# Performance work log

Hardware: AMD Instinct MI355X
Metric: run time of the kernel (lower is better)

## Reference

```python
import jax, jax.numpy as jnp
import numpy as np

N_CLASSES = 10


def setup_inputs() -> dict:
    key = jax.random.key(0)
    k1, k2, k3 = jax.random.split(key, 3)
    x_test = jax.random.uniform(k1, (2048, 784), dtype=jnp.float32)
    x_train = jax.random.uniform(k2, (50000, 784), dtype=jnp.float32)
    y_train = jax.random.randint(k3, (50000,), 0, N_CLASSES, dtype=jnp.int64)
    return {"x_test": x_test, "x_train": x_train, "y_train": y_train, "k": 5}


def reference(x_test, x_train, y_train, k):
    B = x_test.shape[0]
    xt = x_test.reshape(B, -1)                      # [B, D]
    xdb = x_train.reshape(x_train.shape[0], -1)     # [N, D]
    # similarity: matches on 1s + matches on 0s (binary-pixel Hamming-like score)
    dist_full = xt @ xdb.T + (1.0 - xt) @ (1.0 - xdb).T   # [B, N]
    _, idx = jax.lax.top_k(dist_full, k)            # [B, k] nearest-neighbor indices
    yk = y_train[idx]                               # [B, k] neighbor labels
    # per-row mode vote; argmax over class-count histogram == torch's
    counts = jnp.sum(jax.nn.one_hot(yk, N_CLASSES, dtype=jnp.int32), axis=1)  # [B, C]
    return jnp.argmax(counts, axis=1)
```

## Files before the change

kernel.cpp:

```cpp
#include <hip/hip_runtime.h>
#include <float.h>
#include <stdint.h>

#define D_DIM 784
#define KPADB 832
#define N_TRAIN 50000
#define NPAD 50048
#define B_TEST 2048
#define N_CLASSES 10
#define TOPK 5
#define NBLK 391
#define SEL 8
#define SBIAS 12645136
#define NT 13

typedef __attribute__((ext_vector_type(4))) int int4v;

__device__ inline unsigned umax32(unsigned a, unsigned b) { return a > b ? a : b; }

__device__ inline void ins8(unsigned long long* tk, unsigned long long v) {
    #pragma unroll
    for (int s = 0; s < SEL; ++s) {
        unsigned long long mx = v > tk[s] ? v : tk[s];
        unsigned long long mn = v > tk[s] ? tk[s] : v;
        tk[s] = mx; v = mn;
    }
}

__device__ inline void ins5u(unsigned* tk, unsigned v) {
    #pragma unroll
    for (int s = 0; s < TOPK; ++s) {
        unsigned mx = v > tk[s] ? v : tk[s];
        unsigned mn = v > tk[s] ? tk[s] : v;
        tk[s] = mx; v = mn;
    }
}

#define INSERT5(tvarr, tiarr, CV, CI)                                   \
    {                                                                   \
        float _cv = (CV); int _ci = (CI);                               \
        _Pragma("unroll")                                               \
        for (int _s = 0; _s < TOPK; ++_s) {                             \
            bool _bet = (_cv > tvarr[_s]) ||                            \
                        (_cv == tvarr[_s] && _ci < tiarr[_s]);          \
            float _fv = _bet ? tvarr[_s] : _cv;                         \
            int   _fi = _bet ? tiarr[_s] : _ci;                         \
            tvarr[_s] = _bet ? _cv : tvarr[_s];                         \
            tiarr[_s] = _bet ? _ci : tiarr[_s];                         \
            _cv = _fv; _ci = _fi;                                       \
        }                                                               \
    }

__device__ inline unsigned pack4q(float4 f) {
    int q0 = __float2int_rn(fmaf(f.x, 254.f, -127.f));
    int q1 = __float2int_rn(fmaf(f.y, 254.f, -127.f));
    int q2 = __float2int_rn(fmaf(f.z, 254.f, -127.f));
    int q3 = __float2int_rn(fmaf(f.w, 254.f, -127.f));
    return (unsigned)(q0 & 255) | ((unsigned)(q1 & 255) << 8) |
           ((unsigned)(q2 & 255) << 16) | ((unsigned)(q3 & 255) << 24);
}

__global__ __launch_bounds__(256)
void quant_kernel(const float* __restrict__ xtr, const float* __restrict__ xte,
                  char* __restrict__ Bq, char* __restrict__ Aq) {
    const int blk = blockIdx.x;
    const float* src;
    char* dst;
    int rows_src, row;
    if (blk < NPAD / 4) {
        src = xtr; dst = Bq; rows_src = N_TRAIN;
        row = blk * 4 + (threadIdx.x >> 6);
    } else {
        src = xte; dst = Aq; rows_src = B_TEST;
        row = (blk - NPAD / 4) * 4 + (threadIdx.x >> 6);
        if (row >= B_TEST) return;
    }
    const int lane = threadIdx.x & 63;
    if (lane >= 52) return;
    uint4 w = {0u, 0u, 0u, 0u};
    if (row < rows_src && lane < 49) {
        const float4* p = (const float4*)(src + (size_t)row * D_DIM + lane * 16);
        w.x = pack4q(p[0]);
        w.y = pack4q(p[1]);
        w.z = pack4q(p[2]);
        w.w = pack4q(p[3]);
    }
    *(uint4*)(dst + (size_t)row * KPADB + lane * 16) = w;
}

__global__ __launch_bounds__(256, 4)
void knn_mfma(const char* __restrict__ Aq, const char* __restrict__ Bq,
              unsigned* __restrict__ cval) {
    const int bid = blockIdx.x;
    const int xcd = bid & 7;
    const int sidx = bid >> 3;
    const int st_g = (sidx >> 4) * 8 + xcd;
    const int r16 = sidx & 15;
    const int mblk = (st_g & 3) * 4 + (r16 & 3);
    const int nchunk = (st_g >> 2) * 4 + (r16 >> 2);
    if (nchunk >= NBLK) return;

    __shared__ char lds_raw[39936] __attribute__((aligned(16)));
    unsigned* epi  = (unsigned*)lds_raw;
    unsigned* lval = (unsigned*)(lds_raw + 34816);

    const int tid = threadIdx.x;
    const int w = tid >> 6, lane = tid & 63;
    const int l15 = lane & 15, q = lane >> 4;
    const int mb = mblk * 128, nb = nchunk * 128;
    const int mw = (w & 1) * 64, nw = (w >> 1) * 64;

    const int s_tile = w >> 1, s_half = w & 1;
    const char* sbase = (s_tile == 0) ? (Aq + (size_t)mb * KPADB)
                                      : (Bq + (size_t)nb * KPADB);
    const char* srow = sbase + (size_t)s_half * 64 * KPADB;
    const int ldsw_off = s_tile * 8192 + s_half * 4096;

    int choff[4];
    #pragma unroll
    for (int c = 0; c < 4; ++c) {
        int s = c * 64 + lane;
        int rl = s >> 2;
        int k4 = (s & 3) ^ ((rl >> 1) & 3);
        choff[c] = rl * KPADB + k4 * 16;
    }
    const int ch = (q ^ ((l15 >> 1) & 3)) * 16;
    int aoff[4], boff[4];
    #pragma unroll
    for (int i = 0; i < 4; ++i) {
        aoff[i] = (mw + i * 16 + l15) * 64 + ch;
        boff[i] = (nw + i * 16 + l15) * 64 + ch;
    }

    int4v acc[4][4];
    #pragma unroll
    for (int i = 0; i < 4; ++i)
        #pragma unroll
        for (int j = 0; j < 4; ++j)
            acc[i][j] = (int4v){0, 0, 0, 0};

    #define STAGE_TILE(BUF, KT)                                               \
        {                                                                     \
            char* dst_ = lds_raw + (BUF) * 16384 + ldsw_off;                  \
            _Pragma("unroll")                                                 \
            for (int c_ = 0; c_ < 4; ++c_) {                                  \
                __builtin_amdgcn_global_load_lds(                             \
                    (const __attribute__((address_space(1))) void*)           \
                        (srow + choff[c_] + (KT)),                            \
                    (__attribute__((address_space(3))) void*)(dst_ + c_ * 1024),\
                    16, 0, 0);                                                \
            }                                                                 \
        }

    #define COMPUTE_TILE(BUF)                                                 \
        {                                                                     \
            const char* ab_ = lds_raw + (BUF) * 16384;                        \
            int4v a_[4], b_[4];                                               \
            _Pragma("unroll")                                                 \
            for (int i_ = 0; i_ < 4; ++i_) a_[i_] = *(const int4v*)(ab_ + aoff[i_]); \
            _Pragma("unroll")                                                 \
            for (int j_ = 0; j_ < 4; ++j_) b_[j_] = *(const int4v*)(ab_ + 8192 + boff[j_]); \
            _Pragma("unroll")                                                 \
            for (int i_ = 0; i_ < 4; ++i_)                                    \
                _Pragma("unroll")                                             \
                for (int j_ = 0; j_ < 4; ++j_)                                \
                    acc[i_][j_] = __builtin_amdgcn_mfma_i32_16x16x64_i8(      \
                        a_[i_], b_[j_], acc[i_][j_], 0, 0, 0);                \
        }

    STAGE_TILE(0, 0);
    __syncthreads();
    for (int t = 0; t < NT - 1; ++t) {
        const int cur = t & 1;
        STAGE_TILE(cur ^ 1, (t + 1) * 64);
        __builtin_amdgcn_sched_barrier(0);
        COMPUTE_TILE(cur);
        __syncthreads();
    }
    COMPUTE_TILE(0);

    int okn[4];
    #pragma unroll
    for (int j = 0; j < 4; ++j) okn[j] = (nb + nw + j * 16 + l15 < N_TRAIN);

    for (int h = 0; h < 2; ++h) {
        __syncthreads();
        if ((w & 1) == h) {
            #pragma unroll
            for (int i = 0; i < 4; ++i) {
                int r = i * 16 + q * 4;
                #pragma unroll
                for (int j = 0; j < 4; ++j) {
                    int col = nw + j * 16 + l15;
                    uint4 kv;
                    if (okn[j]) {
                        int4v s = acc[i][j];
                        kv.x = ((unsigned)(s.x + SBIAS) << 7) | (unsigned)col;
                        kv.y = ((unsigned)(s.y + SBIAS) << 7) | (unsigned)col;
                        kv.z = ((unsigned)(s.z + SBIAS) << 7) | (unsigned)col;
                        kv.w = ((unsigned)(s.w + SBIAS) << 7) | (unsigned)col;
                    } else {
                        kv.x = kv.y = kv.z = kv.w = (unsigned)col;
                    }
                    *(uint4*)(epi + col * 68 + r) = kv;
                }
            }
        }
        __syncthreads();
        {
            int r = tid & 63, qq = tid >> 6;
            const unsigned* ebase = epi + (qq * 32) * 68 + r;
            unsigned tv5[TOPK] = {0u, 0u, 0u, 0u, 0u};
            #pragma unroll
            for (int c = 0; c < 32; ++c) ins5u(tv5, ebase[c * 68]);
            #pragma unroll
            for (int s = 0; s < TOPK; ++s) lval[(r * 4 + qq) * TOPK + s] = tv5[s];
        }
        __syncthreads();
        if (tid < 64) {
            unsigned tv[TOPK] = {0u, 0u, 0u, 0u, 0u};
            for (int qq = 0; qq < 4; ++qq)
                #pragma unroll
                for (int s = 0; s < TOPK; ++s) {
                    unsigned cv = lval[(tid * 4 + qq) * TOPK + s];
                    if (cv > tv[TOPK - 1]) ins5u(tv, cv);
                }
            int grow = mb + h * 64 + tid;
            size_t base = ((size_t)grow * NBLK + nchunk) * TOPK;
            #pragma unroll
            for (int s = 0; s < TOPK; ++s) cval[base + s] = tv[s];
        }
    }
    #undef STAGE_TILE
    #undef COMPUTE_TILE
}

__global__ __launch_bounds__(256)
void knn_final(const unsigned* __restrict__ cval,
               const float* __restrict__ xt, const float* __restrict__ xtr,
               const int* __restrict__ y, int* __restrict__ out) {
    __shared__ unsigned long long sv[256][SEL];
    __shared__ double cs[SEL];
    __shared__ int    cn[SEL];
    const int b = blockIdx.x;
    const int t = threadIdx.x;

    unsigned long long tk[SEL];
    #pragma unroll
    for (int s = 0; s < SEL; ++s) tk[s] = 0ull;

    const unsigned* row = cval + (size_t)b * (NBLK * TOPK);
    for (int e = t; e < NBLK * TOPK; e += 256) {
        unsigned v = row[e];
        int chunk = e / TOPK;
        unsigned n = (unsigned)chunk * 128u + (v & 127u);
        unsigned long long v64 = ((unsigned long long)v << 16) | n;
        if (v64 > tk[SEL - 1]) ins8(tk, v64);
    }
    #pragma unroll
    for (int s = 0; s < SEL; ++s) sv[t][s] = tk[s];
    __syncthreads();

    for (int off = 128; off >= 1; off >>= 1) {
        if (t < off) {
            if (sv[t + off][0] > tk[SEL - 1]) {
                #pragma unroll
                for (int s = 0; s < SEL; ++s) {
                    unsigned long long v = sv[t + off][s];
                    if (v > tk[SEL - 1]) ins8(tk, v);
                }
                #pragma unroll
                for (int s = 0; s < SEL; ++s) sv[t][s] = tk[s];
            }
        }
        __syncthreads();
    }

    const int w = t >> 6, lane = t & 63, half = lane >> 5, hl = lane & 31;
    const int c = w * 2 + half;
    {
        int n = (int)(sv[0][c] & 0xFFFFull);
        double dot = 0.0, rs = 0.0;
        if (n < N_TRAIN) {
            const float4* pa = (const float4*)(xt + (size_t)b * D_DIM);
            const float4* pb = (const float4*)(xtr + (size_t)n * D_DIM);
            #pragma unroll
            for (int jj = 0; jj < 7; ++jj) {
                int j = hl + jj * 32;
                if (j < 196) {
                    float4 a = pa[j], bb = pb[j];
                    dot += (double)a.x * bb.x + (double)a.y * bb.y +
                           (double)a.z * bb.z + (double)a.w * bb.w;
                    rs  += (double)bb.x + (double)bb.y + (double)bb.z + (double)bb.w;
                }
            }
        }
        #pragma unroll
        for (int off = 16; off > 0; off >>= 1) {
            dot += __shfl_down(dot, off, 32);
            rs  += __shfl_down(rs, off, 32);
        }
        if (hl == 0) {
            cs[c] = (n < N_TRAIN) ? (2.0 * dot - rs) : -1.0e300;
            cn[c] = n;
        }
    }
    __syncthreads();

    if (t == 0) {
        double bv[TOPK]; int bi[TOPK];
        #pragma unroll
        for (int s = 0; s < TOPK; ++s) { bv[s] = -1.0e300; bi[s] = 0x7fffffff; }
        for (int cc = 0; cc < SEL; ++cc) {
            double cv = cs[cc]; int ci = cn[cc];
            #pragma unroll
            for (int s = 0; s < TOPK; ++s) {
                bool bet = (cv > bv[s]) || (cv == bv[s] && ci < bi[s]);
                double fv = bet ? bv[s] : cv;
                int    fi = bet ? bi[s] : ci;
                bv[s] = bet ? cv : bv[s];
                bi[s] = bet ? ci : bi[s];
                cv = fv; ci = fi;
            }
        }
        int lab[TOPK];
        #pragma unroll
        for (int s = 0; s < TOPK; ++s) lab[s] = y[bi[s]];
        int best_c = 0, best_cnt = -1;
        #pragma unroll
        for (int cc = 0; cc < N_CLASSES; ++cc) {
            int cnt = 0;
            #pragma unroll
            for (int s = 0; s < TOPK; ++s) cnt += (lab[s] == cc) ? 1 : 0;
            if (cnt > best_cnt) { best_cnt = cnt; best_c = cc; }
        }
        out[b] = best_c;
    }
}

#define FBM 64
#define FBN 64
#define FBK 16
#define FNCH 32
#define FCHUNK 1600

__global__ __launch_bounds__(256)
void rowsum_kernel(const float* __restrict__ x, float* __restrict__ s) {
    int row = blockIdx.x * 4 + (threadIdx.x >> 6);
    int lane = threadIdx.x & 63;
    if (row >= N_TRAIN) return;
    const float* p = x + (size_t)row * D_DIM;
    float acc = 0.f;
    for (int i = lane; i < D_DIM; i += 64) acc += p[i];
    #pragma unroll
    for (int off = 32; off > 0; off >>= 1) acc += __shfl_down(acc, off, 64);
    if (lane == 0) s[row] = acc;
}

__global__ __launch_bounds__(256)
void knn_phaseA_fb(const float* __restrict__ xt, const float* __restrict__ xtr,
                   const float* __restrict__ strain,
                   float* __restrict__ cval, int* __restrict__ cidx) {
    __shared__ float As[FBK][FBM + 4];
    __shared__ float Bs[FBK][FBN + 4];
    __shared__ float lv[FBM][16][TOPK];
    __shared__ int   li[FBM][16][TOPK];

    const int tid = threadIdx.x;
    const int tx = tid & 15, ty = tid >> 4;
    const int b0 = blockIdx.x * FBM;
    const int chunk = blockIdx.y;
    const int n_base = chunk * FCHUNK;
    const int lrow = tid >> 2;
    const int lk4  = (tid & 3) * 4;

    float tv[4][TOPK]; int ti[4][TOPK];
    #pragma unroll
    for (int i = 0; i < 4; ++i)
        #pragma unroll
        for (int s = 0; s < TOPK; ++s) { tv[i][s] = -FLT_MAX; ti[i][s] = 0x7fffffff; }

    for (int nt = 0; nt < FCHUNK; nt += FBN) {
        const int n0 = n_base + nt;
        double accd[4][4];
        #pragma unroll
        for (int i = 0; i < 4; ++i)
            #pragma unroll
            for (int j = 0; j < 4; ++j) accd[i][j] = 0.0;

        for (int kt = 0; kt < D_DIM; kt += FBK) {
            float4 av = *(const float4*)(xt + (size_t)(b0 + lrow) * D_DIM + kt + lk4);
            As[lk4 + 0][lrow] = av.x; As[lk4 + 1][lrow] = av.y;
            As[lk4 + 2][lrow] = av.z; As[lk4 + 3][lrow] = av.w;
            int nr = n0 + lrow;
            float4 bv = make_float4(0.f, 0.f, 0.f, 0.f);
            if (nr < N_TRAIN) bv = *(const float4*)(xtr + (size_t)nr * D_DIM + kt + lk4);
            Bs[lk4 + 0][lrow] = bv.x; Bs[lk4 + 1][lrow] = bv.y;
            Bs[lk4 + 2][lrow] = bv.z; Bs[lk4 + 3][lrow] = bv.w;
            __syncthreads();

            float accf[4][4] = {{0.f}};
            #pragma unroll
            for (int k = 0; k < FBK; ++k) {
                float a[4], b[4];
                #pragma unroll
                for (int i = 0; i < 4; ++i) a[i] = As[k][ty * 4 + i];
                #pragma unroll
                for (int j = 0; j < 4; ++j) b[j] = Bs[k][tx * 4 + j];
                #pragma unroll
                for (int i = 0; i < 4; ++i)
                    #pragma unroll
                    for (int j = 0; j < 4; ++j) accf[i][j] += a[i] * b[j];
            }
            #pragma unroll
            for (int i = 0; i < 4; ++i)
                #pragma unroll
                for (int j = 0; j < 4; ++j) accd[i][j] += (double)accf[i][j];
            __syncthreads();
        }

        #pragma unroll
        for (int j = 0; j < 4; ++j) {
            int n = n0 + tx * 4 + j;
            if (n < N_TRAIN) {
                float sn = strain[n];
                #pragma unroll
                for (int i = 0; i < 4; ++i) {
                    float sc = (float)(2.0 * accd[i][j] - (double)sn);
                    if (sc > tv[i][TOPK - 1] ||
                        (sc == tv[i][TOPK - 1] && n < ti[i][TOPK - 1])) {
                        INSERT5(tv[i], ti[i], sc, n);
                    }
                }
            }
        }
    }

    #pragma unroll
    for (int i = 0; i < 4; ++i)
        #pragma unroll
        for (int s = 0; s < TOPK; ++s) {
            lv[ty * 4 + i][tx][s] = tv[i][s];
            li[ty * 4 + i][tx][s] = ti[i][s];
        }
    __syncthreads();

    if (tid < FBM) {
        float bv5[TOPK]; int bi5[TOPK];
        #pragma unroll
        for (int s = 0; s < TOPK; ++s) { bv5[s] = -FLT_MAX; bi5[s] = 0x7fffffff; }
        for (int tt = 0; tt < 16; ++tt)
            #pragma unroll
            for (int s = 0; s < TOPK; ++s) {
                float cv = lv[tid][tt][s]; int ci = li[tid][tt][s];
                if (cv > bv5[TOPK - 1] || (cv == bv5[TOPK - 1] && ci < bi5[TOPK - 1])) {
                    INSERT5(bv5, bi5, cv, ci);
                }
            }
        size_t base = ((size_t)(b0 + tid) * FNCH + chunk) * TOPK;
        #pragma unroll
        for (int s = 0; s < TOPK; ++s) { cval[base + s] = bv5[s]; cidx[base + s] = bi5[s]; }
    }
}

__global__ __launch_bounds__(256)
void knn_phaseB_fb(const float* __restrict__ cval, const int* __restrict__ cidx,
                   const int* __restrict__ y, int* __restrict__ out) {
    int b = blockIdx.x * blockDim.x + threadIdx.x;
    if (b >= B_TEST) return;
    const float* v = cval + (size_t)b * FNCH * TOPK;
    const int* ix = cidx + (size_t)b * FNCH * TOPK;
    float bv5[TOPK]; int bi5[TOPK];
    #pragma unroll
    for (int s = 0; s < TOPK; ++s) { bv5[s] = -FLT_MAX; bi5[s] = 0x7fffffff; }
    for (int tt = 0; tt < FNCH * TOPK; ++tt) {
        float cv = v[tt]; int ci = ix[tt];
        if (cv > bv5[TOPK - 1] || (cv == bv5[TOPK - 1] && ci < bi5[TOPK - 1])) {
            INSERT5(bv5, bi5, cv, ci);
        }
    }
    int lab[TOPK];
    #pragma unroll
    for (int s = 0; s < TOPK; ++s) lab[s] = y[bi5[s]];
    int best_c = 0, best_cnt = -1;
    #pragma unroll
    for (int cc = 0; cc < N_CLASSES; ++cc) {
        int cnt = 0;
        #pragma unroll
        for (int s = 0; s < TOPK; ++s) cnt += (lab[s] == cc) ? 1 : 0;
        if (cnt > best_cnt) { best_cnt = cnt; best_c = cc; }
    }
    out[b] = best_c;
}

extern "C" void kernel_launch(void* const* d_in, const int* in_sizes, int n_in,
                              void* d_out, int out_size, void* d_ws, size_t ws_size,
                              hipStream_t stream) {
    const float* x_test  = (const float*)d_in[0];
    const float* x_train = (const float*)d_in[1];
    const int*   y_train = (const int*)d_in[2];
    int* out = (int*)d_out;

    const size_t sz_Bq  = (size_t)NPAD * KPADB;
    const size_t off_Aq = sz_Bq;
    const size_t sz_Aq  = (size_t)B_TEST * KPADB;
    const size_t off_cv = off_Aq + sz_Aq;
    const size_t sz_cv  = (size_t)B_TEST * NBLK * TOPK * 4;
    const size_t need   = off_cv + sz_cv;

    char* ws = (char*)d_ws;

    if (ws_size >= need) {
        char* Bq = ws;
        char* Aq = ws + off_Aq;
        unsigned* cval = (unsigned*)(ws + off_cv);

        quant_kernel<<<NPAD / 4 + B_TEST / 4, 256, 0, stream>>>(
            x_train, x_test, Bq, Aq);

        knn_mfma<<<6272, 256, 0, stream>>>(Aq, Bq, cval);

        knn_final<<<B_TEST, 256, 0, stream>>>(cval, x_test, x_train, y_train, out);
    } else {
        float* strain = (float*)ws;
        rowsum_kernel<<<N_TRAIN / 4, 256, 0, stream>>>(x_train, strain);
        float* cval = (float*)(ws + 200192);
        int*   cidx = (int*)(ws + 200192 + (size_t)B_TEST * FNCH * TOPK * 4);

        dim3 gridA(B_TEST / FBM, FNCH);
        knn_phaseA_fb<<<gridA, 256, 0, stream>>>(x_test, x_train, strain, cval, cidx);
        knn_phaseB_fb<<<(B_TEST + 255) / 256, 256, 0, stream>>>(cval, cidx, y_train, out);
    }
}
```

Measured before the change: 390.3 us.

## Load MFMA operands directly from global into registers, drop LDS staging

Replaces the LDS double-buffered global_load_lds staging with direct per-lane global loads into register double buffers (aX/bX, aY/bY) feeding the int8 MFMAs, fully unrolling the K loop. Launch bounds occupancy hint is lowered from 4 to 3 to allow more registers for the extra operand buffers. This removes LDS traffic and the per-tile barriers, but each wave now fetches its A/B rows from global/L2 itself, so data is no longer shared across waves. That raises global load volume and exposes latency.

Result: slower. 480.5 us (+23.1%).

```diff
diff --git a/kernel.cpp b/kernel.cpp
--- a/kernel.cpp
+++ b/kernel.cpp
@@ -88,7 +88,7 @@
     *(uint4*)(dst + (size_t)row * KPADB + lane * 16) = w;
 }
 
-__global__ __launch_bounds__(256, 4)
+__global__ __launch_bounds__(256, 3)
 void knn_mfma(const char* __restrict__ Aq, const char* __restrict__ Bq,
               unsigned* __restrict__ cval) {
     const int bid = blockIdx.x;
@@ -110,26 +110,12 @@
     const int mb = mblk * 128, nb = nchunk * 128;
     const int mw = (w & 1) * 64, nw = (w >> 1) * 64;
 
-    const int s_tile = w >> 1, s_half = w & 1;
-    const char* sbase = (s_tile == 0) ? (Aq + (size_t)mb * KPADB)
-                                      : (Bq + (size_t)nb * KPADB);
-    const char* srow = sbase + (size_t)s_half * 64 * KPADB;
-    const int ldsw_off = s_tile * 8192 + s_half * 4096;
-
-    int choff[4];
-    #pragma unroll
-    for (int c = 0; c < 4; ++c) {
-        int s = c * 64 + lane;
-        int rl = s >> 2;
-        int k4 = (s & 3) ^ ((rl >> 1) & 3);
-        choff[c] = rl * KPADB + k4 * 16;
-    }
-    const int ch = (q ^ ((l15 >> 1) & 3)) * 16;
-    int aoff[4], boff[4];
+    const char* apt[4];
+    const char* bpt[4];
     #pragma unroll
     for (int i = 0; i < 4; ++i) {
-        aoff[i] = (mw + i * 16 + l15) * 64 + ch;
-        boff[i] = (nw + i * 16 + l15) * 64 + ch;
+        apt[i] = Aq + (size_t)(mb + mw + i * 16 + l15) * KPADB + q * 16;
+        bpt[i] = Bq + (size_t)(nb + nw + i * 16 + l15) * KPADB + q * 16;
     }
 
     int4v acc[4][4];
@@ -139,45 +125,37 @@
         for (int j = 0; j < 4; ++j)
             acc[i][j] = (int4v){0, 0, 0, 0};
 
-    #define STAGE_TILE(BUF, KT)                                               \
+    #define LD8(DA, DB, KT)                                                   \
         {                                                                     \
-            char* dst_ = lds_raw + (BUF) * 16384 + ldsw_off;                  \
             _Pragma("unroll")                                                 \
-            for (int c_ = 0; c_ < 4; ++c_) {                                  \
-                __builtin_amdgcn_global_load_lds(                             \
-                    (const __attribute__((address_space(1))) void*)           \
-                        (srow + choff[c_] + (KT)),                            \
-                    (__attribute__((address_space(3))) void*)(dst_ + c_ * 1024),\
-                    16, 0, 0);                                                \
-            }                                                                 \
-        }
-
-    #define COMPUTE_TILE(BUF)                                                 \
+            for (int i_ = 0; i_ < 4; ++i_) DA[i_] = *(const int4v*)(apt[i_] + (KT)); \
+            _Pragma("unroll")                                                 \
+            for (int j_ = 0; j_ < 4; ++j_) DB[j_] = *(const int4v*)(bpt[j_] + (KT)); \
+        }
+    #define FMA16(SA, SB)                                                     \
         {                                                                     \
-            const char* ab_ = lds_raw + (BUF) * 16384;                        \
-            int4v a_[4], b_[4];                                               \
-            _Pragma("unroll")                                                 \
-            for (int i_ = 0; i_ < 4; ++i_) a_[i_] = *(const int4v*)(ab_ + aoff[i_]); \
-            _Pragma("unroll")                                                 \
-            for (int j_ = 0; j_ < 4; ++j_) b_[j_] = *(const int4v*)(ab_ + 8192 + boff[j_]); \
             _Pragma("unroll")                                                 \
             for (int i_ = 0; i_ < 4; ++i_)                                    \
                 _Pragma("unroll")                                             \
                 for (int j_ = 0; j_ < 4; ++j_)                                \
                     acc[i_][j_] = __builtin_amdgcn_mfma_i32_16x16x64_i8(      \
-                        a_[i_], b_[j_], acc[i_][j_], 0, 0, 0);                \
-        }
-
-    STAGE_TILE(0, 0);
-    __syncthreads();
-    for (int t = 0; t < NT - 1; ++t) {
-        const int cur = t & 1;
-        STAGE_TILE(cur ^ 1, (t + 1) * 64);
-        __builtin_amdgcn_sched_barrier(0);
-        COMPUTE_TILE(cur);
-        __syncthreads();
-    }
-    COMPUTE_TILE(0);
+                        SA[i_], SB[j_], acc[i_][j_], 0, 0, 0);                \
+        }
+
+    {
+        int4v aX[4], bX[4], aY[4], bY[4];
+        LD8(aX, bX, 0);
+        #pragma unroll
+        for (int t = 0; t < NT - 1; t += 2) {
+            LD8(aY, bY, (t + 1) * 64);
+            FMA16(aX, bX);
+            LD8(aX, bX, (t + 2) * 64);
+            FMA16(aY, bY);
+        }
+        FMA16(aX, bX);
+    }
+    #undef LD8
+    #undef FMA16
 
     int okn[4];
     #pragma unroll
@@ -231,8 +209,6 @@
             for (int s = 0; s < TOPK; ++s) cval[base + s] = tv[s];
         }
     }
-    #undef STAGE_TILE
-    #undef COMPUTE_TILE
 }
 
 __global__ __launch_bounds__(256)
```

## Triple-buffer MFMA K-loop with explicit vmcnt waits and dense quant threads

Applied to the files above, without the earlier changes.

Replaces the double-buffered int8 MFMA K-loop with a three-stage LDS ring, prefetching two tiles ahead, using explicit vmcnt waits and raw barriers, and raising wave priority around the MFMA burst. LDS grows to 48KB and launch bounds drop to 3 blocks per CU, trading occupancy for deeper load/compute overlap. The quantization kernel is reorganised so every thread handles one 16-byte chunk, removing the idle lanes of the old 64-lane-per-row mapping.

Result: no change. 394.0 us (+0.9%).

```diff
diff --git a/kernel.cpp b/kernel.cpp
--- a/kernel.cpp
+++ b/kernel.cpp
@@ -13,6 +13,7 @@
 #define SEL 8
 #define SBIAS 12645136
 #define NT 13
+#define RCHUNK 52
 
 typedef __attribute__((ext_vector_type(4))) int int4v;
 
@@ -63,32 +64,30 @@
 __global__ __launch_bounds__(256)
 void quant_kernel(const float* __restrict__ xtr, const float* __restrict__ xte,
                   char* __restrict__ Bq, char* __restrict__ Aq) {
-    const int blk = blockIdx.x;
+    unsigned c = blockIdx.x * 256 + threadIdx.x;
+    unsigned row = c / RCHUNK;
+    unsigned wc  = c - row * RCHUNK;
     const float* src;
     char* dst;
-    int rows_src, row;
-    if (blk < NPAD / 4) {
+    unsigned rows_src;
+    if (row < NPAD) {
         src = xtr; dst = Bq; rows_src = N_TRAIN;
-        row = blk * 4 + (threadIdx.x >> 6);
     } else {
+        row -= NPAD;
         src = xte; dst = Aq; rows_src = B_TEST;
-        row = (blk - NPAD / 4) * 4 + (threadIdx.x >> 6);
-        if (row >= B_TEST) return;
-    }
-    const int lane = threadIdx.x & 63;
-    if (lane >= 52) return;
+    }
     uint4 w = {0u, 0u, 0u, 0u};
-    if (row < rows_src && lane < 49) {
-        const float4* p = (const float4*)(src + (size_t)row * D_DIM + lane * 16);
+    if (row < rows_src && wc < 49) {
+        const float4* p = (const float4*)(src + (size_t)row * D_DIM + wc * 16);
         w.x = pack4q(p[0]);
         w.y = pack4q(p[1]);
         w.z = pack4q(p[2]);
         w.w = pack4q(p[3]);
     }
-    *(uint4*)(dst + (size_t)row * KPADB + lane * 16) = w;
-}
-
-__global__ __launch_bounds__(256, 4)
+    *(uint4*)(dst + (size_t)row * KPADB + wc * 16) = w;
+}
+
+__global__ __launch_bounds__(256, 3)
 void knn_mfma(const char* __restrict__ Aq, const char* __restrict__ Bq,
               unsigned* __restrict__ cval) {
     const int bid = blockIdx.x;
@@ -100,7 +99,7 @@
     const int nchunk = (st_g >> 2) * 4 + (r16 >> 2);
     if (nchunk >= NBLK) return;
 
-    __shared__ char lds_raw[39936] __attribute__((aligned(16)));
+    __shared__ char lds_raw[49152] __attribute__((aligned(16)));
     unsigned* epi  = (unsigned*)lds_raw;
     unsigned* lval = (unsigned*)(lds_raw + 34816);
 
@@ -139,45 +138,70 @@
         for (int j = 0; j < 4; ++j)
             acc[i][j] = (int4v){0, 0, 0, 0};
 
-    #define STAGE_TILE(BUF, KT)                                               \
+    #define ISSUE(T, BT)                                                      \
         {                                                                     \
-            char* dst_ = lds_raw + (BUF) * 16384 + ldsw_off;                  \
+            char* db_ = lds_raw + (BT) * 16384 + ldsw_off;                    \
             _Pragma("unroll")                                                 \
             for (int c_ = 0; c_ < 4; ++c_) {                                  \
                 __builtin_amdgcn_global_load_lds(                             \
                     (const __attribute__((address_space(1))) void*)           \
-                        (srow + choff[c_] + (KT)),                            \
-                    (__attribute__((address_space(3))) void*)(dst_ + c_ * 1024),\
+                        (srow + choff[c_] + (T) * 64),                        \
+                    (__attribute__((address_space(3))) void*)(db_ + c_ * 1024),\
                     16, 0, 0);                                                \
             }                                                                 \
         }
 
-    #define COMPUTE_TILE(BUF)                                                 \
+    #define WAITB(N)                                                          \
+        asm volatile("s_waitcnt vmcnt(" #N ")" ::: "memory");                 \
+        __builtin_amdgcn_sched_barrier(0);                                    \
+        __builtin_amdgcn_s_barrier();                                         \
+        __builtin_amdgcn_sched_barrier(0);
+
+    #define COMP(BT)                                                          \
         {                                                                     \
-            const char* ab_ = lds_raw + (BUF) * 16384;                        \
+            const char* ab_ = lds_raw + (BT) * 16384;                         \
             int4v a_[4], b_[4];                                               \
             _Pragma("unroll")                                                 \
             for (int i_ = 0; i_ < 4; ++i_) a_[i_] = *(const int4v*)(ab_ + aoff[i_]); \
             _Pragma("unroll")                                                 \
             for (int j_ = 0; j_ < 4; ++j_) b_[j_] = *(const int4v*)(ab_ + 8192 + boff[j_]); \
+            __builtin_amdgcn_s_setprio(1);                                    \
             _Pragma("unroll")                                                 \
             for (int i_ = 0; i_ < 4; ++i_)                                    \
                 _Pragma("unroll")                                             \
                 for (int j_ = 0; j_ < 4; ++j_)                                \
                     acc[i_][j_] = __builtin_amdgcn_mfma_i32_16x16x64_i8(      \
                         a_[i_], b_[j_], acc[i_][j_], 0, 0, 0);                \
-        }
-
-    STAGE_TILE(0, 0);
-    __syncthreads();
-    for (int t = 0; t < NT - 1; ++t) {
-        const int cur = t & 1;
-        STAGE_TILE(cur ^ 1, (t + 1) * 64);
+            __builtin_amdgcn_s_setprio(0);                                    \
+        }
+
+    ISSUE(0, 0);
+    __builtin_amdgcn_sched_barrier(0);
+    ISSUE(1, 1);
+    __builtin_amdgcn_sched_barrier(0);
+    ISSUE(2, 2);
+    __builtin_amdgcn_sched_barrier(0);
+
+    int bt = 0;
+    for (int t = 0; t < NT - 3; ++t) {
+        WAITB(8)
+        COMP(bt)
         __builtin_amdgcn_sched_barrier(0);
-        COMPUTE_TILE(cur);
-        __syncthreads();
-    }
-    COMPUTE_TILE(0);
+        __builtin_amdgcn_s_barrier();
+        __builtin_amdgcn_sched_barrier(0);
+        ISSUE(t + 3, bt)
+        __builtin_amdgcn_sched_barrier(0);
+        bt = (bt == 2) ? 0 : bt + 1;
+    }
+    WAITB(8)
+    COMP(1)
+    WAITB(4)
+    COMP(2)
+    WAITB(0)
+    COMP(0)
+    #undef ISSUE
+    #undef WAITB
+    #undef COMP
 
     int okn[4];
     #pragma unroll
@@ -231,8 +255,6 @@
             for (int s = 0; s < TOPK; ++s) cval[base + s] = tv[s];
         }
     }
-    #undef STAGE_TILE
-    #undef COMPUTE_TILE
 }
 
 __global__ __launch_bounds__(256)
@@ -515,8 +537,8 @@
         char* Aq = ws + off_Aq;
         unsigned* cval = (unsigned*)(ws + off_cv);
 
-        quant_kernel<<<NPAD / 4 + B_TEST / 4, 256, 0, stream>>>(
-            x_train, x_test, Bq, Aq);
+        const int qblocks = ((NPAD + B_TEST) * RCHUNK) / 256;
+        quant_kernel<<<qblocks, 256, 0, stream>>>(x_train, x_test, Bq, Aq);
 
         knn_mfma<<<6272, 256, 0, stream>>>(Aq, Bq, cval);
 
```
